# Kernel optimization log

Measured on AMD Instinct MI355X. Metric: run time of the kernel, lower is better.

The kernel has to match this reference:

```python
import jax, jax.numpy as jnp
import numpy as np

B, CIN, COUT, H, W, K, WDIM = 16, 512, 512, 32, 32, 3, 512


def setup_inputs() -> dict:
    key = jax.random.key(0)
    k0, k1, k2, k3 = jax.random.split(key, 4)
    return {
        "image": jax.random.normal(k0, (B, CIN, H, W), dtype=jnp.float32),
        "w_latent": jax.random.normal(k1, (B, WDIM), dtype=jnp.float32),
        "dense_kernel": jax.random.normal(k2, (WDIM, CIN), dtype=jnp.float32) * 0.02,
        "dense_bias": jnp.zeros((CIN,), dtype=jnp.float32),
        "conv_weights": jax.random.normal(k3, (K, K, CIN, COUT), dtype=jnp.float32),
    }


def reference(image, w_latent, dense_kernel, dense_bias, conv_weights):
    # style scale from Dense(w) -> [B, Cin]
    style = w_latent @ dense_kernel + dense_bias
    # per-sample modulated weights: [B, kh, kw, Cin, Cout]
    w = conv_weights[None] * style[:, None, None, :, None]
    # faithful to source: reduce over axes [2,3,4] (kw, Cin, Cout) -> [B, kh];
    # no epsilon added (source defines but never uses self.epsilon)
    denom = jax.lax.rsqrt(jnp.sum(w * w, axis=(2, 3, 4)))
    w = w * denom[:, :, None, None, None]
    b, cin, h, wid = image.shape
    cout = w.shape[-1]
    # batch-as-groups trick: [1, B*Cin, H, W] conv [kh, kw, Cin, B*Cout] with groups=B
    eff_img = image.reshape(1, b * cin, h, wid)
    eff_filt = jnp.transpose(w, (1, 2, 3, 0, 4)).reshape(w.shape[1], w.shape[2], cin, b * cout)
    out = jax.lax.conv_general_dilated(
        eff_img, eff_filt,
        window_strides=(1, 1), padding="SAME",
        dimension_numbers=("NCHW", "HWIO", "NCHW"),
        feature_group_count=b,
    )
    return out.reshape(b, cout, out.shape[2], out.shape[3])
```

## Files before the change

kernel.cpp:

```cpp
#include <hip/hip_runtime.h>
#include <hip/hip_bf16.h>


typedef short short8 __attribute__((ext_vector_type(8)));
typedef float f32x4 __attribute__((ext_vector_type(4)));

__device__ __forceinline__ ushort bf16_rtne(float f) {
    unsigned u = __float_as_uint(f);
    unsigned r = u + 0x7fffu + ((u >> 16) & 1u);
    return (ushort)(r >> 16);
}
__device__ __forceinline__ float bf16_up(ushort h) {
    return __uint_as_float(((unsigned)h) << 16);
}
__device__ __forceinline__ void gld16(const void* g, void* l) {
    __builtin_amdgcn_global_load_lds(
        (const __attribute__((address_space(1))) unsigned int*)g,
        (__attribute__((address_space(3))) unsigned int*)l, 16, 0, 0);
}

__global__ __launch_bounds__(256) void style_kernel(const float* __restrict__ wl,
                                                    const float* __restrict__ dk,
                                                    const float* __restrict__ bias,
                                                    float* __restrict__ style) {
    __shared__ float wsh[512];
    __shared__ float red[4][64];
    const int b = blockIdx.y, c0 = blockIdx.x * 64, t = threadIdx.x;
    for (int i = t; i < 512; i += 256) wsh[i] = wl[b * 512 + i];
    __syncthreads();
    const int c = c0 + (t & 63), kq = (t >> 6) * 128;
    float acc = 0.f;
    #pragma unroll 8
    for (int k = 0; k < 128; ++k)
        acc = fmaf(wsh[kq + k], dk[(size_t)(kq + k) * 512 + c], acc);
    red[t >> 6][t & 63] = acc;
    __syncthreads();
    if (t < 64)
        style[b * 512 + c0 + t] =
            red[0][t] + red[1][t] + red[2][t] + red[3][t] + bias[c0 + t];
}

__global__ void denom_kernel(const float* __restrict__ S,
                             const float* __restrict__ style,
                             float* __restrict__ dn) {
    int bid = blockIdx.x;
    int b = bid / 3, kh = bid % 3;
    int lane = threadIdx.x;
    float acc = 0.f;
    for (int c = lane; c < 512; c += 64) {
        float s = style[b * 512 + c];
        acc = fmaf(S[kh * 512 + c], s * s, acc);
    }
    #pragma unroll
    for (int off = 32; off; off >>= 1) acc += __shfl_down(acc, off);
    if (lane == 0) dn[bid] = rsqrtf(acc);
}

__global__ __launch_bounds__(256) void wsplit_kernel(const float* __restrict__ cw,
                                                     ushort* __restrict__ wt3,
                                                     float* __restrict__ S) {
    __shared__ ushort hs[64][72];
    __shared__ ushort ls[64][72];
    int t = threadIdx.x;
    int k0 = blockIdx.x * 64, c0 = blockIdx.y * 64;
    int col = t & 63;
    int rq = t >> 6;
    const int khw = k0 >> 9;
    const int kh = khw >= 6 ? 2 : (khw >= 3 ? 1 : 0);
    #pragma unroll
    for (int i = 0; i < 16; ++i) {
        int kr = rq * 16 + i;
        float v = cw[(size_t)(k0 + kr) * 512 + c0 + col];
        ushort hh = bf16_rtne(v);
        ushort ll = bf16_rtne(v - bf16_up(hh));
        hs[col][kr] = hh;
        ls[col][kr] = ll;
        float sq = v * v;
        #pragma unroll
        for (int off = 32; off; off >>= 1) sq += __shfl_down(sq, off);
        if ((t & 63) == 0)
            atomicAdd(&S[kh * 512 + ((k0 & 511) + kr)], sq);
    }
    __syncthreads();
    int r = t >> 2, kq = (t & 3) << 4;
    int cout = c0 + r;
    int k = k0 + kq;
    size_t o = ((size_t)((cout >> 7) * 144 + (k >> 5)) * 2 + ((cout >> 6) & 1)) * 4096
             + (size_t)((cout >> 4) & 3) * 1024
             + (size_t)(((k >> 3) & 3) * 16 + (cout & 15)) * 8;
    *(uint4*)&wt3[o]       = *(const uint4*)&hs[r][kq];
    *(uint4*)&wt3[o + 128] = *(const uint4*)&hs[r][kq + 8];
    *(uint4*)&wt3[o + 512] = *(const uint4*)&ls[r][kq];
    *(uint4*)&wt3[o + 640] = *(const uint4*)&ls[r][kq + 8];
}

__global__ __launch_bounds__(256) void isplit_kernel(const float* __restrict__ img,
                                                     const float* __restrict__ style,
                                                     ushort* __restrict__ ihi,
                                                     ushort* __restrict__ ilo) {
    const int b = blockIdx.y, yp = blockIdx.x, t = threadIdx.x;
    const size_t rowbase = (size_t)(b * 34 + yp) * 34 * 512;
    uint4 z = {0u, 0u, 0u, 0u};
    if (yp == 0 || yp == 33) {
        for (int i = t; i < 2176; i += 256) {
            ((uint4*)(ihi + rowbase))[i] = z;
            ((uint4*)(ilo + rowbase))[i] = z;
        }
        return;
    }
    if (t < 64) {
        ((uint4*)(ihi + rowbase))[t] = z;
        ((uint4*)(ilo + rowbase))[t] = z;
        ((uint4*)(ihi + rowbase + 33 * 512))[t] = z;
        ((uint4*)(ilo + rowbase + 33 * 512))[t] = z;
    }
    const int y = yp - 1;
    __shared__ float buf[64][33];
    const int ci = t >> 5, x = t & 31;
    const int xo = t >> 3, cs = (t & 7) * 8;
    const int xp = xo + 1;
    const int sig = (xp >> 1) & 3;
    const size_t o_sw = rowbase + (size_t)xp * 512 + (cs & 32)
                      + (size_t)((((cs >> 3) & 3) ^ sig) << 3);
    for (int c0 = 0; c0 < 512; c0 += 64) {
        __syncthreads();
        #pragma unroll
        for (int i = 0; i < 8; ++i) {
            int cin = c0 + ci + i * 8;
            float v = img[((size_t)(b * 512 + cin) * 32 + y) * 32 + x] *
                      style[b * 512 + cin];
            buf[ci + i * 8][x] = v;
        }
        __syncthreads();
        union { ushort u[8]; uint4 v; } hb, lb;
        #pragma unroll
        for (int i = 0; i < 8; ++i) {
            float v = buf[cs + i][xo];
            ushort hh = bf16_rtne(v);
            hb.u[i] = hh;
            lb.u[i] = bf16_rtne(v - bf16_up(hh));
        }
        *(uint4*)&ihi[o_sw + c0] = hb.v;
        *(uint4*)&ilo[o_sw + c0] = lb.v;
    }
}

__global__ __launch_bounds__(256, 2) void conv_gemm(
    const ushort* __restrict__ wt3,
    const ushort* __restrict__ ihh,
    const ushort* __restrict__ ihl,
    const float*  __restrict__ dn,
    float* __restrict__ out)
{
    __shared__ ushort Ih[2][128][32];
    __shared__ ushort Io[2][128][32];

    const int tid  = threadIdx.x;
    const int lane = tid & 63;
    const int wid  = tid >> 6;

    const int g   = blockIdx.x;
    const int swz = ((g & 7) << 6) | (g >> 3);
    const int coutblk = swz >> 7;
    const int pixblk  = swz & 127;
    const int b        = pixblk >> 3;
    const int pix_base = (pixblk & 7) << 7;

    const int wr = (wid >> 1) * 64;
    const int wc = (wid & 1) * 64;
    const int rl  = lane & 15;
    const int kgB = (lane >> 4) << 3;

    const int r0 = wid << 5;
    const int rA = r0 + (lane >> 2);
    const int rB = rA + 16;
    const int ck = (lane & 3) << 3;
    const size_t ibase = (size_t)b * 34 * 34 * 512;
    const int gpA = pix_base + rA, gpB = pix_base + rB;
    const size_t pAoff = ibase + (size_t)((gpA >> 5) * 34 + (gpA & 31)) * 512 + ck;
    const size_t pBoff = ibase + (size_t)((gpB >> 5) * 34 + (gpB & 31)) * 512 + ck;

    const int half = wid >> 1;
    const ushort* wpBase = wt3 + (size_t)coutblk * 1179648 + (size_t)half * 4096 + lane * 8;

    const float d0 = dn[b * 3 + 0];
    const float d1 = dn[b * 3 + 1];
    const float d2 = dn[b * 3 + 2];

    f32x4 acc[4][4];
    #pragma unroll
    for (int i = 0; i < 4; ++i)
        #pragma unroll
        for (int j = 0; j < 4; ++j) acc[i][j] = (f32x4)0.f;

    short8 wRegA[8], wRegB[8];

    gld16(ihh + pAoff, &Ih[0][r0][0]);
    gld16(ihh + pBoff, &Ih[0][r0 + 16][0]);
    gld16(ihl + pAoff, &Io[0][r0][0]);
    gld16(ihl + pBoff, &Io[0][r0 + 16][0]);
    #pragma unroll
    for (int j = 0; j < 8; ++j) wRegA[j] = *(const short8*)(wpBase + j * 512);
    __syncthreads();

#define CONV_BODY(STEP, CUR, WUSE, WPRE)                                          \
    {                                                                             \
        const int step = (STEP);                                                  \
        const int khw  = step >> 4;                                               \
        const int kh   = khw >= 6 ? 2 : (khw >= 3 ? 1 : 0);                       \
        const int kw   = khw - kh * 3;                                            \
        if (step < 143) {                                                         \
            const int s1   = step + 1;                                            \
            const int khw1 = s1 >> 4;                                             \
            const int kh1  = khw1 >= 6 ? 2 : (khw1 >= 3 ? 1 : 0);                 \
            const int kw1  = khw1 - kh1 * 3;                                      \
            const int soff1 = (kh1 * 34 + kw1) * 512 + ((s1 << 5) & 511);         \
            gld16(ihh + pAoff + soff1, &Ih[(CUR) ^ 1][r0][0]);                    \
            gld16(ihh + pBoff + soff1, &Ih[(CUR) ^ 1][r0 + 16][0]);               \
            gld16(ihl + pAoff + soff1, &Io[(CUR) ^ 1][r0][0]);                    \
            gld16(ihl + pBoff + soff1, &Io[(CUR) ^ 1][r0 + 16][0]);               \
            const ushort* wsrc = wpBase + (size_t)s1 * 8192;                      \
            _Pragma("unroll")                                                     \
            for (int j = 0; j < 8; ++j) WPRE[j] = *(const short8*)(wsrc + j * 512);\
        }                                                                         \
        const int sig = (((rl + kw) >> 1) & 3) << 3;                              \
        const int colr = kgB ^ sig;                                               \
        short8 ia[4], il[4];                                                      \
        _Pragma("unroll")                                                         \
        for (int ni = 0; ni < 4; ++ni) {                                          \
            const int row = wc + ni * 16 + rl;                                    \
            ia[ni] = *(const short8*)&Ih[CUR][row][colr];                         \
            il[ni] = *(const short8*)&Io[CUR][row][colr];                         \
        }                                                                         \
        _Pragma("unroll")                                                         \
        for (int mi = 0; mi < 4; ++mi) {                                          \
            _Pragma("unroll")                                                     \
            for (int ni = 0; ni < 4; ++ni) {                                      \
                acc[mi][ni] = __builtin_amdgcn_mfma_f32_16x16x32_bf16(            \
                    WUSE[mi * 2 + 0], ia[ni], acc[mi][ni], 0, 0, 0);              \
                acc[mi][ni] = __builtin_amdgcn_mfma_f32_16x16x32_bf16(            \
                    WUSE[mi * 2 + 0], il[ni], acc[mi][ni], 0, 0, 0);              \
                acc[mi][ni] = __builtin_amdgcn_mfma_f32_16x16x32_bf16(            \
                    WUSE[mi * 2 + 1], ia[ni], acc[mi][ni], 0, 0, 0);              \
            }                                                                     \
        }                                                                         \
        if (step == 47 || step == 95) {                                           \
            const float rr = (step == 47) ? (d0 / d1) : (d1 / d2);                \
            _Pragma("unroll")                                                     \
            for (int mi = 0; mi < 4; ++mi)                                        \
                _Pragma("unroll")                                                 \
                for (int ni = 0; ni < 4; ++ni) acc[mi][ni] *= rr;                 \
        }                                                                         \
        __syncthreads();                                                          \
    }

    for (int it = 0; it < 72; ++it) {
        CONV_BODY(2 * it,     0, wRegA, wRegB)
        CONV_BODY(2 * it + 1, 1, wRegB, wRegA)
    }
#undef CONV_BODY

    const int cout_base = coutblk << 7;
    #pragma unroll
    for (int mi = 0; mi < 4; ++mi) {
        const int crow = cout_base + wr + mi * 16 + ((lane >> 4) << 2);
        #pragma unroll
        for (int ni = 0; ni < 4; ++ni) {
            const int ccol = pix_base + wc + ni * 16 + (lane & 15);
            float* op = out + ((size_t)(b << 9) + crow) * 1024 + ccol;
            f32x4 c = acc[mi][ni];
            #pragma unroll
            for (int r = 0; r < 4; ++r)
                op[(size_t)r * 1024] = c[r] * d2;
        }
    }
}

extern "C" void kernel_launch(void* const* d_in, const int* in_sizes, int n_in,
                              void* d_out, int out_size, void* d_ws, size_t ws_size,
                              hipStream_t stream) {
    const float* img  = (const float*)d_in[0];
    const float* wl   = (const float*)d_in[1];
    const float* dk   = (const float*)d_in[2];
    const float* bias = (const float*)d_in[3];
    const float* cw   = (const float*)d_in[4];
    float* out = (float*)d_out;

    float* style = (float*)d_ws;
    float* S     = style + 8192;
    float* dn    = S + 1536;
    ushort* wt3  = (ushort*)((char*)d_ws + 65536);
    ushort* ihi  = wt3 + (size_t)4 * 144 * 8192;
    ushort* ilo  = ihi + (size_t)16 * 34 * 34 * 512;

    hipMemsetAsync(S, 0, 1536 * sizeof(float), stream);
    style_kernel<<<dim3(8, 16), 256, 0, stream>>>(wl, dk, bias, style);
    wsplit_kernel<<<dim3(72, 8), 256, 0, stream>>>(cw, wt3, S);
    denom_kernel<<<48, 64, 0, stream>>>(S, style, dn);
    isplit_kernel<<<dim3(34, 16), 256, 0, stream>>>(img, style, ihi, ilo);

    conv_gemm<<<512, 256, 0, stream>>>(wt3, ihi, ilo, dn, out);
}
```

Baseline: 357.1 us.

## Stage halo input tile once per channel chunk and reuse across nine taps

```diff
diff --git a/kernel.cpp b/kernel.cpp
--- a/kernel.cpp
+++ b/kernel.cpp
@@ -118,10 +118,6 @@
     __shared__ float buf[64][33];
     const int ci = t >> 5, x = t & 31;
     const int xo = t >> 3, cs = (t & 7) * 8;
-    const int xp = xo + 1;
-    const int sig = (xp >> 1) & 3;
-    const size_t o_sw = rowbase + (size_t)xp * 512 + (cs & 32)
-                      + (size_t)((((cs >> 3) & 3) ^ sig) << 3);
     for (int c0 = 0; c0 < 512; c0 += 64) {
         __syncthreads();
         #pragma unroll
@@ -140,8 +136,9 @@
             hb.u[i] = hh;
             lb.u[i] = bf16_rtne(v - bf16_up(hh));
         }
-        *(uint4*)&ihi[o_sw + c0] = hb.v;
-        *(uint4*)&ilo[o_sw + c0] = lb.v;
+        size_t o = rowbase + (size_t)(xo + 1) * 512 + c0 + cs;
+        *(uint4*)&ihi[o] = hb.v;
+        *(uint4*)&ilo[o] = lb.v;
     }
 }
 
@@ -152,8 +149,8 @@
     const float*  __restrict__ dn,
     float* __restrict__ out)
 {
-    __shared__ ushort Ih[2][128][32];
-    __shared__ ushort Io[2][128][32];
+    __shared__ ushort Hs[2][224][32];
+    __shared__ ushort Ls[2][224][32];
 
     const int tid  = threadIdx.x;
     const int lane = tid & 63;
@@ -165,27 +162,21 @@
     const int pixblk  = swz & 127;
     const int b        = pixblk >> 3;
     const int pix_base = (pixblk & 7) << 7;
-
-    const int wr = (wid >> 1) * 64;
-    const int wc = (wid & 1) * 64;
+    const int Y0       = pix_base >> 5;
+
+    const int wr  = (wid >> 1) * 64;
+    const int wc  = (wid & 1) * 64;
     const int rl  = lane & 15;
     const int kgB = (lane >> 4) << 3;
 
-    const int r0 = wid << 5;
-    const int rA = r0 + (lane >> 2);
-    const int rB = rA + 16;
-    const int ck = (lane & 3) << 3;
     const size_t ibase = (size_t)b * 34 * 34 * 512;
-    const int gpA = pix_base + rA, gpB = pix_base + rB;
-    const size_t pAoff = ibase + (size_t)((gpA >> 5) * 34 + (gpA & 31)) * 512 + ck;
-    const size_t pBoff = ibase + (size_t)((gpB >> 5) * 34 + (gpB & 31)) * 512 + ck;
-
     const int half = wid >> 1;
     const ushort* wpBase = wt3 + (size_t)coutblk * 1179648 + (size_t)half * 4096 + lane * 8;
 
     const float d0 = dn[b * 3 + 0];
     const float d1 = dn[b * 3 + 1];
     const float d2 = dn[b * 3 + 2];
+    const float r01 = d0 / d1, r12 = d1 / d2, r20 = d2 / d0;
 
     f32x4 acc[4][4];
     #pragma unroll
@@ -193,72 +184,91 @@
         #pragma unroll
         for (int j = 0; j < 4; ++j) acc[i][j] = (f32x4)0.f;
 
-    short8 wRegA[8], wRegB[8];
-
-    gld16(ihh + pAoff, &Ih[0][r0][0]);
-    gld16(ihh + pBoff, &Ih[0][r0 + 16][0]);
-    gld16(ihl + pAoff, &Io[0][r0][0]);
-    gld16(ihl + pBoff, &Io[0][r0 + 16][0]);
-    #pragma unroll
-    for (int j = 0; j < 8; ++j) wRegA[j] = *(const short8*)(wpBase + j * 512);
+    short8 wA[8], wB[8];
+
+#define STAGE(CEV, NB)                                                         \
+    { _Pragma("unroll")                                                        \
+      for (int kk = 0; kk < 7; ++kk) {                                         \
+        const int kc = wid + kk * 4;                                           \
+        const int tsel = kc & 1;                                               \
+        const int rb = (kc >> 1) << 4;                                         \
+        const int r  = rb + (lane >> 2);                                       \
+        const int yr = r / 36, xp = r - yr * 36;                               \
+        const int yp = min(Y0 + yr, 33), xpc = min(xp, 33);                    \
+        const ushort* src = (tsel ? ihl : ihh) + ibase                         \
+            + ((size_t)(yp * 34 + xpc) << 9) + ((CEV) << 5)                    \
+            + ((lane & 3) << 3);                                               \
+        ushort* dst = tsel ? &Ls[NB][rb][0] : &Hs[NB][rb][0];                  \
+        gld16(src, dst);                                                       \
+      } }
+
+#define RESCALE(RR)                                                            \
+    { _Pragma("unroll")                                                        \
+      for (int mi = 0; mi < 4; ++mi)                                           \
+        _Pragma("unroll")                                                      \
+        for (int ni = 0; ni < 4; ++ni) acc[mi][ni] *= (RR); }
+
+#define STEP(S9, CEV, WUSE, WPRE, BUF)                                         \
+    {                                                                          \
+        const int kh = (S9) / 3, kw = (S9) % 3;                                \
+        const int ns = ((S9) == 8) ? 0 : (S9) + 1;                             \
+        const int nc = ((S9) == 8) ? (CEV) + 1 : (CEV);                        \
+        if (nc < 16) {                                                         \
+            const ushort* wsrc = wpBase + (size_t)(ns * 16 + nc) * 8192;       \
+            _Pragma("unroll")                                                  \
+            for (int j = 0; j < 8; ++j)                                        \
+                WPRE[j] = *(const short8*)(wsrc + j * 512);                    \
+        }                                                                      \
+        short8 ia[4], il[4];                                                   \
+        _Pragma("unroll")                                                      \
+        for (int ni = 0; ni < 4; ++ni) {                                       \
+            const int R0 = ((wc >> 5) + (ni >> 1) + kh) * 36                   \
+                         + (ni & 1) * 16 + kw;                                 \
+            ia[ni] = *(const short8*)&Hs[BUF][R0 + rl][kgB];                   \
+            il[ni] = *(const short8*)&Ls[BUF][R0 + rl][kgB];                   \
+        }                                                                      \
+        _Pragma("unroll")                                                      \
+        for (int mi = 0; mi < 4; ++mi) {                                       \
+            _Pragma("unroll")                                                  \
+            for (int ni = 0; ni < 4; ++ni) {                                   \
+                acc[mi][ni] = __builtin_amdgcn_mfma_f32_16x16x32_bf16(         \
+                    WUSE[mi * 2 + 0], ia[ni], acc[mi][ni], 0, 0, 0);           \
+                acc[mi][ni] = __builtin_amdgcn_mfma_f32_16x16x32_bf16(         \
+                    WUSE[mi * 2 + 0], il[ni], acc[mi][ni], 0, 0, 0);           \
+                acc[mi][ni] = __builtin_amdgcn_mfma_f32_16x16x32_bf16(         \
+                    WUSE[mi * 2 + 1], ia[ni], acc[mi][ni], 0, 0, 0);           \
+            }                                                                  \
+        }                                                                      \
+    }
+
+#define EVENT(CEV, BUF, NB, W0, W1)                                            \
+    {                                                                          \
+        if ((CEV) < 15) STAGE((CEV) + 1, NB)                                   \
+        STEP(0, CEV, W0, W1, BUF) STEP(1, CEV, W1, W0, BUF)                    \
+        STEP(2, CEV, W0, W1, BUF)                                              \
+        RESCALE(r01)                                                           \
+        STEP(3, CEV, W1, W0, BUF) STEP(4, CEV, W0, W1, BUF)                    \
+        STEP(5, CEV, W1, W0, BUF)                                              \
+        RESCALE(r12)                                                           \
+        STEP(6, CEV, W0, W1, BUF) STEP(7, CEV, W1, W0, BUF)                    \
+        STEP(8, CEV, W0, W1, BUF)                                              \
+        if ((CEV) < 15) RESCALE(r20)                                           \
+        __syncthreads();                                                       \
+    }
+
+    STAGE(0, 0)
+    #pragma unroll
+    for (int j = 0; j < 8; ++j) wA[j] = *(const short8*)(wpBase + j * 512);
     __syncthreads();
 
-#define CONV_BODY(STEP, CUR, WUSE, WPRE)                                          \
-    {                                                                             \
-        const int step = (STEP);                                                  \
-        const int khw  = step >> 4;                                               \
-        const int kh   = khw >= 6 ? 2 : (khw >= 3 ? 1 : 0);                       \
-        const int kw   = khw - kh * 3;                                            \
-        if (step < 143) {                                                         \
-            const int s1   = step + 1;                                            \
-            const int khw1 = s1 >> 4;                                             \
-            const int kh1  = khw1 >= 6 ? 2 : (khw1 >= 3 ? 1 : 0);                 \
-            const int kw1  = khw1 - kh1 * 3;                                      \
-            const int soff1 = (kh1 * 34 + kw1) * 512 + ((s1 << 5) & 511);         \
-            gld16(ihh + pAoff + soff1, &Ih[(CUR) ^ 1][r0][0]);                    \
-            gld16(ihh + pBoff + soff1, &Ih[(CUR) ^ 1][r0 + 16][0]);               \
-            gld16(ihl + pAoff + soff1, &Io[(CUR) ^ 1][r0][0]);                    \
-            gld16(ihl + pBoff + soff1, &Io[(CUR) ^ 1][r0 + 16][0]);               \
-            const ushort* wsrc = wpBase + (size_t)s1 * 8192;                      \
-            _Pragma("unroll")                                                     \
-            for (int j = 0; j < 8; ++j) WPRE[j] = *(const short8*)(wsrc + j * 512);\
-        }                                                                         \
-        const int sig = (((rl + kw) >> 1) & 3) << 3;                              \
-        const int colr = kgB ^ sig;                                               \
-        short8 ia[4], il[4];                                                      \
-        _Pragma("unroll")                                                         \
-        for (int ni = 0; ni < 4; ++ni) {                                          \
-            const int row = wc + ni * 16 + rl;                                    \
-            ia[ni] = *(const short8*)&Ih[CUR][row][colr];                         \
-            il[ni] = *(const short8*)&Io[CUR][row][colr];                         \
-        }                                                                         \
-        _Pragma("unroll")                                                         \
-        for (int mi = 0; mi < 4; ++mi) {                                          \
-            _Pragma("unroll")                                                     \
-            for (int ni = 0; ni < 4; ++ni) {                                      \
-                acc[mi][ni] = __builtin_amdgcn_mfma_f32_16x16x32_bf16(            \
-                    WUSE[mi * 2 + 0], ia[ni], acc[mi][ni], 0, 0, 0);              \
-                acc[mi][ni] = __builtin_amdgcn_mfma_f32_16x16x32_bf16(            \
-                    WUSE[mi * 2 + 0], il[ni], acc[mi][ni], 0, 0, 0);              \
-                acc[mi][ni] = __builtin_amdgcn_mfma_f32_16x16x32_bf16(            \
-                    WUSE[mi * 2 + 1], ia[ni], acc[mi][ni], 0, 0, 0);              \
-            }                                                                     \
-        }                                                                         \
-        if (step == 47 || step == 95) {                                           \
-            const float rr = (step == 47) ? (d0 / d1) : (d1 / d2);                \
-            _Pragma("unroll")                                                     \
-            for (int mi = 0; mi < 4; ++mi)                                        \
-                _Pragma("unroll")                                                 \
-                for (int ni = 0; ni < 4; ++ni) acc[mi][ni] *= rr;                 \
-        }                                                                         \
-        __syncthreads();                                                          \
-    }
-
-    for (int it = 0; it < 72; ++it) {
-        CONV_BODY(2 * it,     0, wRegA, wRegB)
-        CONV_BODY(2 * it + 1, 1, wRegB, wRegA)
-    }
-#undef CONV_BODY
+    for (int cp = 0; cp < 8; ++cp) {
+        EVENT(2 * cp,     0, 1, wA, wB)
+        EVENT(2 * cp + 1, 1, 0, wB, wA)
+    }
+#undef EVENT
+#undef STEP
+#undef RESCALE
+#undef STAGE
 
     const int cout_base = coutblk << 7;
     #pragma unroll
```

After: 329.1 us. 7.8% less time.
